# Optimization experiments

Measured on AMD Instinct MI355X. Metric: run time of the kernel, lower is better.

The kernel has to match this reference:

```python
import jax, jax.numpy as jnp
import numpy as np

SEQ_LEN = 1024
BATCH = 256
HIDDEN = 100
OUT = 1

L_FILTER = [-0.0106, 0.0329, 0.0308, -0.187, -0.028, 0.6309, 0.7148, 0.2304]
H_FILTER = [-0.2304, 0.7148, -0.6309, -0.028, 0.187, 0.0308, -0.0329, -0.0106]


def _create_W(P, is_l, rng):
    filt = L_FILTER if is_l else H_FILTER
    eps = np.min(np.abs(filt))
    W = rng.standard_normal((P, P)) * 0.1 * eps
    for i in range(P):
        for k, j in enumerate(range(i, min(i + len(filt), P))):
            W[i, j] = filt[k]
    return jnp.asarray(W, dtype=jnp.float32)


def setup_inputs() -> dict:
    key = jax.random.key(0)
    ks = jax.random.split(key, 16)
    rng = np.random.default_rng(0)
    T, H = SEQ_LEN, HIDDEN
    s = 1.0 / np.sqrt(H)

    def lstm_params(k):
        k1, k2, k3 = jax.random.split(k, 3)
        Wih = jax.random.uniform(k1, (4 * H, 1), jnp.float32, -s, s)
        Whh = jax.random.uniform(k2, (4 * H, H), jnp.float32, -s, s)
        b = jax.random.uniform(k3, (4 * H,), jnp.float32, -s, s)
        return Wih, Whh, b

    Wih1, Whh1, b1 = lstm_params(ks[0])
    Wih2, Whh2, b2 = lstm_params(ks[1])
    Wih3, Whh3, b3 = lstm_params(ks[2])
    return {
        "x": jax.random.normal(ks[3], (BATCH, T, 1), jnp.float32),
        "W1H": _create_W(T, False, rng),
        "b1H": jax.random.uniform(ks[4], (T,), jnp.float32, -1 / np.sqrt(T), 1 / np.sqrt(T)),
        "W1L": _create_W(T, True, rng),
        "b1L": jax.random.uniform(ks[5], (T,), jnp.float32, -1 / np.sqrt(T), 1 / np.sqrt(T)),
        "W2H": _create_W(T // 2, False, rng),
        "b2H": jax.random.uniform(ks[6], (T // 2,), jnp.float32, -1 / np.sqrt(T // 2), 1 / np.sqrt(T // 2)),
        "W2L": _create_W(T // 2, True, rng),
        "b2L": jax.random.uniform(ks[7], (T // 2,), jnp.float32, -1 / np.sqrt(T // 2), 1 / np.sqrt(T // 2)),
        "Wih1": Wih1, "Whh1": Whh1, "b1": b1,
        "Wih2": Wih2, "Whh2": Whh2, "b2": b2,
        "Wih3": Wih3, "Whh3": Whh3, "b3": b3,
        "Wout": jax.random.uniform(ks[8], (OUT, H), jnp.float32, -s, s),
        "bout": jax.random.uniform(ks[9], (OUT,), jnp.float32, -s, s),
    }


def _avgpool2(x):  # [B, L] -> [B, L//2], AvgPool1d(kernel=2, stride=2)
    B, L = x.shape
    return x.reshape(B, L // 2, 2).mean(-1)


def _lstm(x, Wih, Whh, b):
    # x: [B, T, 1]; torch LSTM gate order i, f, g, o; h0 = c0 = 0
    H = Whh.shape[1]
    gx = jnp.einsum('bti,gi->btg', x, Wih) + b  # [B, T, 4H]

    def step(carry, g):
        h, c = carry
        z = g + h @ Whh.T
        i, f, gg, o = jnp.split(z, 4, axis=-1)
        c = jax.nn.sigmoid(f) * c + jax.nn.sigmoid(i) * jnp.tanh(gg)
        h = jax.nn.sigmoid(o) * jnp.tanh(c)
        return (h, c), h

    B = x.shape[0]
    h0 = jnp.zeros((B, H), x.dtype)
    _, hs = jax.lax.scan(step, (h0, h0), jnp.swapaxes(gx, 0, 1))
    return jnp.swapaxes(hs, 0, 1)  # [B, T, H]


def reference(x, W1H, b1H, W1L, b1L, W2H, b2H, W2L, b2L,
              Wih1, Whh1, b1, Wih2, Whh2, b2, Wih3, Whh3, b3, Wout, bout):
    inp = x[:, :, -1]  # [B, T]
    ah1 = jax.nn.sigmoid(inp @ W1H.T + b1H)
    al1 = jax.nn.sigmoid(inp @ W1L.T + b1L)
    xh1 = _avgpool2(ah1)  # [B, T/2]
    xl1 = _avgpool2(al1)  # [B, T/2]
    ah2 = jax.nn.sigmoid(xl1 @ W2H.T + b2H)
    al2 = jax.nn.sigmoid(xl1 @ W2L.T + b2L)
    xh2 = _avgpool2(ah2)  # [B, T/4]
    xl2 = _avgpool2(al2)  # [B, T/4]
    s1 = _lstm(xh1[..., None], Wih1, Whh1, b1)
    s2 = _lstm(xh2[..., None], Wih2, Whh2, b2)
    s3 = _lstm(xl2[..., None], Wih3, Whh3, b3)
    cat = jnp.concatenate([s1, s2, s3], axis=1)  # [B, T, H]
    out = cat @ Wout.T + bout  # [B, T, OUT]
    return out[:, -1, :]
```

## Files before the change

kernel.cpp:

```cpp
#include <hip/hip_runtime.h>
#include <math.h>

typedef __bf16 bf16x8 __attribute__((ext_vector_type(8)));
typedef _Float16 f16x8 __attribute__((ext_vector_type(8)));
typedef _Float16 f16x4 __attribute__((ext_vector_type(4)));
typedef float f32x4 __attribute__((ext_vector_type(4)));

__device__ __forceinline__ unsigned short f2bf(float f) {
  unsigned int u = __builtin_bit_cast(unsigned int, f);
  u += 0x7fffu + ((u >> 16) & 1u);
  return (unsigned short)(u >> 16);
}
__device__ __forceinline__ unsigned int pack2bf(float a, float b) {
  return (unsigned int)f2bf(a) | ((unsigned int)f2bf(b) << 16);
}

#define GK_PAD2 72
template <int WFP32, int XFP32>
__global__ __launch_bounds__(256) void gemm_mfma_sig_pool(
    const void* __restrict__ Wv, const float* __restrict__ bias,
    const void* __restrict__ Xv, void* __restrict__ Y,
    int K, int Np, int out_bf16) {
  __shared__ unsigned short Wt[64][GK_PAD2];
  __shared__ unsigned short Xt[16][GK_PAD2];
  const int tid = threadIdx.x;
  const int i_base = blockIdx.x * 64;
  const int b_base = blockIdx.y * 16;
  const int srow = tid >> 2, sseg = tid & 3;
  const int xr = tid >> 4, xs = tid & 15;
  const int wv = tid >> 6, lane = tid & 63;
  const int L15 = lane & 15, q = lane >> 4;

  const float* Wf = (const float*)Wv;
  const float* Xf = (const float*)Xv;
  const unsigned short* Wh = (const unsigned short*)Wv;
  const unsigned short* Xh = (const unsigned short*)Xv;

  float4 wf[2][4];
  uint4 wh[2][2];
  float4 xf[2];
  uint2 xh2[2];

#define LOADW(S, KO)                                                          \
  do {                                                                        \
    if (WFP32) {                                                              \
      _Pragma("unroll") for (int j = 0; j < 4; j++)                           \
          wf[S][j] = *(const float4*)&Wf[(size_t)(i_base + srow) * K + (KO) + \
                                         sseg * 16 + 4 * j];                  \
    } else {                                                                  \
      _Pragma("unroll") for (int j = 0; j < 2; j++)                           \
          wh[S][j] = *(const uint4*)&Wh[(size_t)(i_base + srow) * K + (KO) +  \
                                        sseg * 16 + 8 * j];                   \
    }                                                                         \
  } while (0)

#define LOADX(S, KO)                                                          \
  do {                                                                        \
    if (XFP32) {                                                              \
      xf[S] = *(const float4*)&Xf[(size_t)(b_base + xr) * K + (KO) + xs * 4]; \
    } else {                                                                  \
      xh2[S] = *(const uint2*)&Xh[(size_t)(b_base + xr) * K + (KO) + xs * 4]; \
    }                                                                         \
  } while (0)

#define STAGEW(S)                                                             \
  do {                                                                        \
    if (WFP32) {                                                              \
      uint4 p0 = {pack2bf(wf[S][0].x, wf[S][0].y),                            \
                  pack2bf(wf[S][0].z, wf[S][0].w),                            \
                  pack2bf(wf[S][1].x, wf[S][1].y),                            \
                  pack2bf(wf[S][1].z, wf[S][1].w)};                           \
      uint4 p1 = {pack2bf(wf[S][2].x, wf[S][2].y),                            \
                  pack2bf(wf[S][2].z, wf[S][2].w),                            \
                  pack2bf(wf[S][3].x, wf[S][3].y),                            \
                  pack2bf(wf[S][3].z, wf[S][3].w)};                           \
      *(uint4*)&Wt[srow][sseg * 16] = p0;                                     \
      *(uint4*)&Wt[srow][sseg * 16 + 8] = p1;                                 \
    } else {                                                                  \
      *(uint4*)&Wt[srow][sseg * 16] = wh[S][0];                               \
      *(uint4*)&Wt[srow][sseg * 16 + 8] = wh[S][1];                           \
    }                                                                         \
  } while (0)

#define STAGEX(S)                                                             \
  do {                                                                        \
    if (XFP32) {                                                              \
      uint2 p = {pack2bf(xf[S].x, xf[S].y), pack2bf(xf[S].z, xf[S].w)};       \
      *(uint2*)&Xt[xr][xs * 4] = p;                                           \
    } else {                                                                  \
      *(uint2*)&Xt[xr][xs * 4] = xh2[S];                                      \
    }                                                                         \
  } while (0)

#define DOMFMA                                                                \
  do {                                                                        \
    _Pragma("unroll") for (int kt = 0; kt < 2; kt++) {                        \
      bf16x8 a = *(const bf16x8*)&Wt[wv * 16 + L15][kt * 32 + q * 8];         \
      bf16x8 b = *(const bf16x8*)&Xt[L15][kt * 32 + q * 8];                   \
      acc = __builtin_amdgcn_mfma_f32_16x16x32_bf16(a, b, acc, 0, 0, 0);      \
    }                                                                         \
  } while (0)

  f32x4 acc = {};
  LOADW(0, 0);
  LOADX(0, 0);
  for (int k0 = 0; k0 < K; k0 += 128) {
    LOADW(1, k0 + 64);
    LOADX(1, k0 + 64);
    STAGEW(0);
    STAGEX(0);
    __syncthreads();
    DOMFMA;
    __syncthreads();
    if (k0 + 128 < K) {
      LOADW(0, k0 + 128);
      LOADX(0, k0 + 128);
    }
    STAGEW(1);
    STAGEX(1);
    __syncthreads();
    DOMFMA;
    __syncthreads();
  }
#undef LOADW
#undef LOADX
#undef STAGEW
#undef STAGEX
#undef DOMFMA

  {
    const int nrow = i_base + 16 * wv + q * 4;
    const float bi0 = bias[nrow], bi1 = bias[nrow + 1];
    const float bi2 = bias[nrow + 2], bi3 = bias[nrow + 3];
    const int b = b_base + L15;
    const float a0 = __builtin_amdgcn_rcpf(1.f + __expf(-(acc[0] + bi0)));
    const float a1 = __builtin_amdgcn_rcpf(1.f + __expf(-(acc[1] + bi1)));
    const float a2 = __builtin_amdgcn_rcpf(1.f + __expf(-(acc[2] + bi2)));
    const float a3 = __builtin_amdgcn_rcpf(1.f + __expf(-(acc[3] + bi3)));
    const float p0 = 0.5f * (a0 + a1), p1 = 0.5f * (a2 + a3);
    const int pidx = nrow >> 1;
    if (out_bf16) {
      *(unsigned int*)&((unsigned short*)Y)[(size_t)b * Np + pidx] = pack2bf(p0, p1);
    } else {
      *(float2*)&((float*)Y)[(size_t)b * Np + pidx] = make_float2(p0, p1);
    }
  }
}

#define LOG2E 1.44269504f
#define TWOL2E 2.88539008f
__global__ __launch_bounds__(256) void prep_whh(
    const float* __restrict__ Whh, const float* __restrict__ b3,
    _Float16* __restrict__ P) {
  const int idx = blockIdx.x * 256 + threadIdx.x;
  if (idx >= 400 * 16) return;
  const int row = idx >> 4, ch = idx & 15;
  const int hid = row >> 2, gate = row & 3;
  const int src = gate * 100 + hid;
  const float s = (gate == 2) ? TWOL2E : LOG2E;
  f16x8 v;
#pragma unroll
  for (int j = 0; j < 8; j++) {
    const int k = ch * 8 + j;
    float f = 0.f;
    if (k < 100) f = Whh[(size_t)src * 100 + k] * s;
    v[j] = (_Float16)f;
  }
  *(f16x8*)&P[(size_t)row * 128 + ch * 8] = v;
}

#define TSTEPS 256

__device__ __forceinline__ float qb0(float x) {
  return __builtin_bit_cast(float, __builtin_amdgcn_mov_dpp(__builtin_bit_cast(int, x), 0x00, 0xf, 0xf, true));
}
__device__ __forceinline__ float qb1(float x) {
  return __builtin_bit_cast(float, __builtin_amdgcn_mov_dpp(__builtin_bit_cast(int, x), 0x55, 0xf, 0xf, true));
}
__device__ __forceinline__ float qb2(float x) {
  return __builtin_bit_cast(float, __builtin_amdgcn_mov_dpp(__builtin_bit_cast(int, x), 0xAA, 0xf, 0xf, true));
}
__device__ __forceinline__ float qb3(float x) {
  return __builtin_bit_cast(float, __builtin_amdgcn_mov_dpp(__builtin_bit_cast(int, x), 0xFF, 0xf, 0xf, true));
}

__global__ __launch_bounds__(512, 2) void lstm_mfma(
    const float* __restrict__ X, const _Float16* __restrict__ P,
    const float* __restrict__ Whh, const float* __restrict__ Wih,
    const float* __restrict__ b3, const float* __restrict__ Wout,
    const float* __restrict__ bout, float* __restrict__ out) {
  const int bat = blockIdx.x;
  const int t = threadIdx.x;
  const int w = t >> 6, lane = t & 63;
  const int quad = lane >> 4, c = lane & 15;
  const int TB = (w == 7) ? 21 : w * 3;
  const int NT = (w == 7) ? 4 : 3;

  __shared__ __align__(16) _Float16 hbuf[2][128];
  __shared__ float xrow[TSTEPS];
  __shared__ float red[128];

  for (int i = t; i < TSTEPS; i += 512) xrow[i] = X[(size_t)bat * TSTEPS + i];
  if (t < 128) { hbuf[0][t] = (_Float16)0.f; hbuf[1][t] = (_Float16)0.f; }

#define LDA(J, KT) const f16x8 A##J##KT = \
    *(const f16x8*)&P[(size_t)((TB + J) * 16 + c) * 128 + (KT) * 32 + quad * 8];
  LDA(0,0) LDA(0,1) LDA(0,2)
  LDA(1,0) LDA(1,1) LDA(1,2)
  LDA(2,0) LDA(2,1) LDA(2,2)
  LDA(3,0) LDA(3,1) LDA(3,2)
#undef LDA

  const bool act = (c < 4 * NT);
  const int J = c >> 2, g = c & 3;
  const int myhid = 4 * (TB + (act ? J : 0)) + quad;
  const int grow = g * 100 + myhid;
  const float sc = (g == 2) ? TWOL2E : LOG2E;
  const float u_ = Wih[grow] * sc;
  const float bz = b3[grow] * sc;
  const float4 wt0 = *(const float4*)&Whh[(size_t)grow * 100 + 96];
  const float4 wt = make_float4(wt0.x * sc, wt0.y * sc, wt0.z * sc, wt0.w * sc);
  const float mm = (g == 2) ? 2.f : 1.f;
  const float dd = (g == 2) ? -1.f : 0.f;
  float cst = 0.f;
  __syncthreads();

#define SIG2(zz) __builtin_amdgcn_rcpf(1.f + __builtin_amdgcn_exp2f(-(zz)))
#define STEPB(HC, HN, XT)                                                      \
  {                                                                            \
    const _Float16* hc = (HC);                                                 \
    const f16x8 B0 = *(const f16x8*)&hc[0 * 32 + quad * 8];                    \
    const f16x8 B1 = *(const f16x8*)&hc[1 * 32 + quad * 8];                    \
    const f16x8 B2 = *(const f16x8*)&hc[2 * 32 + quad * 8];                    \
    f32x4 z0 = {0.f,0.f,0.f,0.f}, z1 = z0, z2 = z0, z3 = z0;                   \
    { f32x4 za = z0, zb = z0;                                                  \
      za = __builtin_amdgcn_mfma_f32_16x16x32_f16(A00, B0, za, 0, 0, 0);       \
      zb = __builtin_amdgcn_mfma_f32_16x16x32_f16(A01, B1, zb, 0, 0, 0);       \
      za = __builtin_amdgcn_mfma_f32_16x16x32_f16(A02, B2, za, 0, 0, 0);       \
      z0 = za + zb; }                                                          \
    { f32x4 za = {0.f,0.f,0.f,0.f}, zb = za;                                   \
      za = __builtin_amdgcn_mfma_f32_16x16x32_f16(A10, B0, za, 0, 0, 0);       \
      zb = __builtin_amdgcn_mfma_f32_16x16x32_f16(A11, B1, zb, 0, 0, 0);       \
      za = __builtin_amdgcn_mfma_f32_16x16x32_f16(A12, B2, za, 0, 0, 0);       \
      z1 = za + zb; }                                                          \
    { f32x4 za = {0.f,0.f,0.f,0.f}, zb = za;                                   \
      za = __builtin_amdgcn_mfma_f32_16x16x32_f16(A20, B0, za, 0, 0, 0);       \
      zb = __builtin_amdgcn_mfma_f32_16x16x32_f16(A21, B1, zb, 0, 0, 0);       \
      za = __builtin_amdgcn_mfma_f32_16x16x32_f16(A22, B2, za, 0, 0, 0);       \
      z2 = za + zb; }                                                          \
    if (w == 7) {                                                              \
      f32x4 za = {0.f,0.f,0.f,0.f}, zb = za;                                   \
      za = __builtin_amdgcn_mfma_f32_16x16x32_f16(A30, B0, za, 0, 0, 0);       \
      zb = __builtin_amdgcn_mfma_f32_16x16x32_f16(A31, B1, zb, 0, 0, 0);       \
      za = __builtin_amdgcn_mfma_f32_16x16x32_f16(A32, B2, za, 0, 0, 0);       \
      z3 = za + zb; }                                                          \
    if (act) {                                                                 \
      const f32x4 zt = (J == 0) ? z0 : (J == 1) ? z1 : (J == 2) ? z2 : z3;     \
      float zs = (g == 0) ? zt[0] : (g == 1) ? zt[1] : (g == 2) ? zt[2] : zt[3];\
      const f16x4 ht = *(const f16x4*)&hc[96];                                 \
      zs = fmaf(wt.x, (float)ht[0], zs);                                       \
      zs = fmaf(wt.y, (float)ht[1], zs);                                       \
      zs = fmaf(wt.z, (float)ht[2], zs);                                       \
      zs = fmaf(wt.w, (float)ht[3], zs);                                       \
      zs = fmaf(u_, (XT), zs + bz);                                            \
      const float a = mm * SIG2(zs) + dd;                                      \
      const float ai = qb0(a), af = qb1(a), ag = qb2(a), ao = qb3(a);          \
      cst = fmaf(af, cst, ai * ag);                                            \
      const float th = 2.f * SIG2(TWOL2E * cst) - 1.f;                         \
      if (g == 0) (HN)[myhid] = (_Float16)(ao * th);                           \
    }                                                                          \
    __syncthreads();                                                           \
  }

  for (int step = 0; step < TSTEPS; step += 2) {
    STEPB(hbuf[0], hbuf[1], xrow[step]);
    STEPB(hbuf[1], hbuf[0], xrow[step + 1]);
  }
#undef STEPB
#undef SIG2

  if (t < 128) {
    float a = 0.f;
    if (t < 100) a = (float)hbuf[0][t] * Wout[t];
    red[t] = a;
  }
  __syncthreads();
  if (t == 0) {
    float s = 0.f;
#pragma unroll
    for (int k = 0; k < 128; k++) s += red[k];
    out[bat] = s + bout[0];
  }
}

extern "C" void kernel_launch(void* const* d_in, const int* in_sizes, int n_in,
                              void* d_out, int out_size, void* d_ws, size_t ws_size,
                              hipStream_t stream) {
  const float* x    = (const float*)d_in[0];
  const float* W1L  = (const float*)d_in[3];
  const float* b1L  = (const float*)d_in[4];
  const float* W2L  = (const float*)d_in[7];
  const float* b2L  = (const float*)d_in[8];
  const float* Wih3 = (const float*)d_in[15];
  const float* Whh3 = (const float*)d_in[16];
  const float* b3   = (const float*)d_in[17];
  const float* Wout = (const float*)d_in[18];
  const float* bout = (const float*)d_in[19];
  float* out = (float*)d_out;

  unsigned short* xl1b = (unsigned short*)d_ws;
  float* xl2 = (float*)(xl1b + (size_t)256 * 512);
  _Float16* P = (_Float16*)(xl2 + (size_t)256 * 256);

  prep_whh<<<25, 256, 0, stream>>>(Whh3, b3, P);
  gemm_mfma_sig_pool<1, 1><<<dim3(16, 16), 256, 0, stream>>>(W1L, b1L, x, xl1b, 1024, 512, 1);
  gemm_mfma_sig_pool<1, 0><<<dim3(8, 16), 256, 0, stream>>>(W2L, b2L, xl1b, xl2, 512, 256, 0);
  lstm_mfma<<<256, 512, 0, stream>>>(xl2, P, Whh3, Wih3, b3, Wout, bout, out);
}
```

Before: 231.1 us.

## Fuse all four kernels into one cooperative kernel with grid syncs

Replaces the four separate launches (Whh prep, two GEMM+sigmoid+pool stages, LSTM) with a single cooperative kernel that separates phases with grid-wide syncs. The GEMM phase now uses 512 threads with a 128-wide K tile and splits K across wave pairs, reducing the partials through shared memory. The aim is to remove launch gaps and inter-kernel drain. In exchange it adds grid.sync costs, limits the grid to what can be co-resident, and idles half the blocks during the second GEMM.

```diff
diff --git a/kernel.cpp b/kernel.cpp
--- a/kernel.cpp
+++ b/kernel.cpp
@@ -1,11 +1,18 @@
 #include <hip/hip_runtime.h>
+#include <hip/hip_cooperative_groups.h>
 #include <math.h>
+
+namespace cg = cooperative_groups;
 
 typedef __bf16 bf16x8 __attribute__((ext_vector_type(8)));
 typedef _Float16 f16x8 __attribute__((ext_vector_type(8)));
 typedef _Float16 f16x4 __attribute__((ext_vector_type(4)));
 typedef float f32x4 __attribute__((ext_vector_type(4)));
 
+#define LOG2E 1.44269504f
+#define TWOL2E 2.88539008f
+#define TSTEPS 256
+
 __device__ __forceinline__ unsigned short f2bf(float f) {
   unsigned int u = __builtin_bit_cast(unsigned int, f);
   u += 0x7fffu + ((u >> 16) & 1u);
@@ -15,43 +22,54 @@
   return (unsigned int)f2bf(a) | ((unsigned int)f2bf(b) << 16);
 }
 
-#define GK_PAD2 72
-template <int WFP32, int XFP32>
-__global__ __launch_bounds__(256) void gemm_mfma_sig_pool(
-    const void* __restrict__ Wv, const float* __restrict__ bias,
+__device__ __forceinline__ float qb0(float x) {
+  return __builtin_bit_cast(float, __builtin_amdgcn_mov_dpp(__builtin_bit_cast(int, x), 0x00, 0xf, 0xf, true));
+}
+__device__ __forceinline__ float qb1(float x) {
+  return __builtin_bit_cast(float, __builtin_amdgcn_mov_dpp(__builtin_bit_cast(int, x), 0x55, 0xf, 0xf, true));
+}
+__device__ __forceinline__ float qb2(float x) {
+  return __builtin_bit_cast(float, __builtin_amdgcn_mov_dpp(__builtin_bit_cast(int, x), 0xAA, 0xf, 0xf, true));
+}
+__device__ __forceinline__ float qb3(float x) {
+  return __builtin_bit_cast(float, __builtin_amdgcn_mov_dpp(__builtin_bit_cast(int, x), 0xFF, 0xf, 0xf, true));
+}
+
+struct SmemG {
+  unsigned short Wt[64][136];
+  unsigned short Xt[16][136];
+  float racc[4][64][4];
+};
+struct SmemL {
+  _Float16 hbuf[2][128];
+  float xrow[TSTEPS];
+  float red[128];
+};
+union SmemU { SmemG g; SmemL l; };
+
+template <int XFP32>
+__device__ __forceinline__ void gemm_phase(
+    const float* __restrict__ Wf, const float* __restrict__ bias,
     const void* __restrict__ Xv, void* __restrict__ Y,
-    int K, int Np, int out_bf16) {
-  __shared__ unsigned short Wt[64][GK_PAD2];
-  __shared__ unsigned short Xt[16][GK_PAD2];
-  const int tid = threadIdx.x;
-  const int i_base = blockIdx.x * 64;
-  const int b_base = blockIdx.y * 16;
-  const int srow = tid >> 2, sseg = tid & 3;
-  const int xr = tid >> 4, xs = tid & 15;
-  const int wv = tid >> 6, lane = tid & 63;
+    const int K, const int Np, const int out_bf16,
+    const int i_base, const int b_base, SmemG* sm, const int tid) {
+  const int srow = tid >> 3, sseg = tid & 7;
+  const int xr = tid >> 5, xs = tid & 31;
+  const int w = tid >> 6, lane = tid & 63;
+  const int rgrp = w >> 1, kg = w & 1;
   const int L15 = lane & 15, q = lane >> 4;
-
-  const float* Wf = (const float*)Wv;
   const float* Xf = (const float*)Xv;
-  const unsigned short* Wh = (const unsigned short*)Wv;
   const unsigned short* Xh = (const unsigned short*)Xv;
 
   float4 wf[2][4];
-  uint4 wh[2][2];
   float4 xf[2];
   uint2 xh2[2];
 
 #define LOADW(S, KO)                                                          \
   do {                                                                        \
-    if (WFP32) {                                                              \
-      _Pragma("unroll") for (int j = 0; j < 4; j++)                           \
-          wf[S][j] = *(const float4*)&Wf[(size_t)(i_base + srow) * K + (KO) + \
-                                         sseg * 16 + 4 * j];                  \
-    } else {                                                                  \
-      _Pragma("unroll") for (int j = 0; j < 2; j++)                           \
-          wh[S][j] = *(const uint4*)&Wh[(size_t)(i_base + srow) * K + (KO) +  \
-                                        sseg * 16 + 8 * j];                   \
-    }                                                                         \
+    _Pragma("unroll") for (int j = 0; j < 4; j++)                             \
+        wf[S][j] = *(const float4*)&Wf[(size_t)(i_base + srow) * K + (KO) +   \
+                                       sseg * 16 + 4 * j];                    \
   } while (0)
 
 #define LOADX(S, KO)                                                          \
@@ -65,56 +83,52 @@
 
 #define STAGEW(S)                                                             \
   do {                                                                        \
-    if (WFP32) {                                                              \
-      uint4 p0 = {pack2bf(wf[S][0].x, wf[S][0].y),                            \
-                  pack2bf(wf[S][0].z, wf[S][0].w),                            \
-                  pack2bf(wf[S][1].x, wf[S][1].y),                            \
-                  pack2bf(wf[S][1].z, wf[S][1].w)};                           \
-      uint4 p1 = {pack2bf(wf[S][2].x, wf[S][2].y),                            \
-                  pack2bf(wf[S][2].z, wf[S][2].w),                            \
-                  pack2bf(wf[S][3].x, wf[S][3].y),                            \
-                  pack2bf(wf[S][3].z, wf[S][3].w)};                           \
-      *(uint4*)&Wt[srow][sseg * 16] = p0;                                     \
-      *(uint4*)&Wt[srow][sseg * 16 + 8] = p1;                                 \
-    } else {                                                                  \
-      *(uint4*)&Wt[srow][sseg * 16] = wh[S][0];                               \
-      *(uint4*)&Wt[srow][sseg * 16 + 8] = wh[S][1];                           \
-    }                                                                         \
+    uint4 p0 = {pack2bf(wf[S][0].x, wf[S][0].y),                              \
+                pack2bf(wf[S][0].z, wf[S][0].w),                              \
+                pack2bf(wf[S][1].x, wf[S][1].y),                              \
+                pack2bf(wf[S][1].z, wf[S][1].w)};                             \
+    uint4 p1 = {pack2bf(wf[S][2].x, wf[S][2].y),                              \
+                pack2bf(wf[S][2].z, wf[S][2].w),                              \
+                pack2bf(wf[S][3].x, wf[S][3].y),                              \
+                pack2bf(wf[S][3].z, wf[S][3].w)};                             \
+    *(uint4*)&sm->Wt[srow][sseg * 16] = p0;                                   \
+    *(uint4*)&sm->Wt[srow][sseg * 16 + 8] = p1;                               \
   } while (0)
 
 #define STAGEX(S)                                                             \
   do {                                                                        \
     if (XFP32) {                                                              \
       uint2 p = {pack2bf(xf[S].x, xf[S].y), pack2bf(xf[S].z, xf[S].w)};       \
-      *(uint2*)&Xt[xr][xs * 4] = p;                                           \
+      *(uint2*)&sm->Xt[xr][xs * 4] = p;                                       \
     } else {                                                                  \
-      *(uint2*)&Xt[xr][xs * 4] = xh2[S];                                      \
+      *(uint2*)&sm->Xt[xr][xs * 4] = xh2[S];                                  \
     }                                                                         \
   } while (0)
 
 #define DOMFMA                                                                \
   do {                                                                        \
-    _Pragma("unroll") for (int kt = 0; kt < 2; kt++) {                        \
-      bf16x8 a = *(const bf16x8*)&Wt[wv * 16 + L15][kt * 32 + q * 8];         \
-      bf16x8 b = *(const bf16x8*)&Xt[L15][kt * 32 + q * 8];                   \
-      acc = __builtin_amdgcn_mfma_f32_16x16x32_bf16(a, b, acc, 0, 0, 0);      \
+    _Pragma("unroll") for (int tki = 0; tki < 2; tki++) {                     \
+      const int kt = kg * 2 + tki;                                            \
+      bf16x8 a = *(const bf16x8*)&sm->Wt[rgrp * 16 + L15][kt * 32 + q * 8];   \
+      bf16x8 bb = *(const bf16x8*)&sm->Xt[L15][kt * 32 + q * 8];              \
+      acc = __builtin_amdgcn_mfma_f32_16x16x32_bf16(a, bb, acc, 0, 0, 0);     \
     }                                                                         \
   } while (0)
 
   f32x4 acc = {};
   LOADW(0, 0);
   LOADX(0, 0);
-  for (int k0 = 0; k0 < K; k0 += 128) {
-    LOADW(1, k0 + 64);
-    LOADX(1, k0 + 64);
+  for (int k0 = 0; k0 < K; k0 += 256) {
+    LOADW(1, k0 + 128);
+    LOADX(1, k0 + 128);
     STAGEW(0);
     STAGEX(0);
     __syncthreads();
     DOMFMA;
     __syncthreads();
-    if (k0 + 128 < K) {
-      LOADW(0, k0 + 128);
-      LOADX(0, k0 + 128);
+    if (k0 + 256 < K) {
+      LOADW(0, k0 + 256);
+      LOADX(0, k0 + 256);
     }
     STAGEW(1);
     STAGEX(1);
@@ -128,8 +142,11 @@
 #undef STAGEX
 #undef DOMFMA
 
-  {
-    const int nrow = i_base + 16 * wv + q * 4;
+  if (kg == 1) *(f32x4*)&sm->racc[rgrp][lane][0] = acc;
+  __syncthreads();
+  if (kg == 0) {
+    acc += *(const f32x4*)&sm->racc[rgrp][lane][0];
+    const int nrow = i_base + rgrp * 16 + q * 4;
     const float bi0 = bias[nrow], bi1 = bias[nrow + 1];
     const float bi2 = bias[nrow + 2], bi3 = bias[nrow + 3];
     const int b = b_base + L15;
@@ -145,85 +162,90 @@
       *(float2*)&((float*)Y)[(size_t)b * Np + pidx] = make_float2(p0, p1);
     }
   }
-}
-
-#define LOG2E 1.44269504f
-#define TWOL2E 2.88539008f
-__global__ __launch_bounds__(256) void prep_whh(
+  __syncthreads();
+}
+
+__global__ __launch_bounds__(512, 2) void fused_all(
+    const float* __restrict__ x, const float* __restrict__ W1L,
+    const float* __restrict__ b1L, const float* __restrict__ W2L,
+    const float* __restrict__ b2L, const float* __restrict__ Wih,
     const float* __restrict__ Whh, const float* __restrict__ b3,
-    _Float16* __restrict__ P) {
-  const int idx = blockIdx.x * 256 + threadIdx.x;
-  if (idx >= 400 * 16) return;
-  const int row = idx >> 4, ch = idx & 15;
-  const int hid = row >> 2, gate = row & 3;
-  const int src = gate * 100 + hid;
-  const float s = (gate == 2) ? TWOL2E : LOG2E;
-  f16x8 v;
+    const float* __restrict__ Wout, const float* __restrict__ bout,
+    unsigned short* __restrict__ xl1b, float* __restrict__ xl2,
+    _Float16* __restrict__ P, float* __restrict__ out) {
+  __shared__ __align__(16) SmemU smem;
+  const int t = threadIdx.x;
+  const int blk = blockIdx.x;
+  cg::grid_group grid = cg::this_grid();
+
+  {
+    const int idx = blk * 512 + t;
+    if (idx < 400 * 16) {
+      const int row = idx >> 4, ch = idx & 15;
+      const int hid = row >> 2, gate = row & 3;
+      const int src = gate * 100 + hid;
+      const float s = (gate == 2) ? TWOL2E : LOG2E;
+      f16x8 v;
 #pragma unroll
-  for (int j = 0; j < 8; j++) {
-    const int k = ch * 8 + j;
-    float f = 0.f;
-    if (k < 100) f = Whh[(size_t)src * 100 + k] * s;
-    v[j] = (_Float16)f;
-  }
-  *(f16x8*)&P[(size_t)row * 128 + ch * 8] = v;
-}
-
-#define TSTEPS 256
-
-__device__ __forceinline__ float qb0(float x) {
-  return __builtin_bit_cast(float, __builtin_amdgcn_mov_dpp(__builtin_bit_cast(int, x), 0x00, 0xf, 0xf, true));
-}
-__device__ __forceinline__ float qb1(float x) {
-  return __builtin_bit_cast(float, __builtin_amdgcn_mov_dpp(__builtin_bit_cast(int, x), 0x55, 0xf, 0xf, true));
-}
-__device__ __forceinline__ float qb2(float x) {
-  return __builtin_bit_cast(float, __builtin_amdgcn_mov_dpp(__builtin_bit_cast(int, x), 0xAA, 0xf, 0xf, true));
-}
-__device__ __forceinline__ float qb3(float x) {
-  return __builtin_bit_cast(float, __builtin_amdgcn_mov_dpp(__builtin_bit_cast(int, x), 0xFF, 0xf, 0xf, true));
-}
-
-__global__ __launch_bounds__(512, 2) void lstm_mfma(
-    const float* __restrict__ X, const _Float16* __restrict__ P,
-    const float* __restrict__ Whh, const float* __restrict__ Wih,
-    const float* __restrict__ b3, const float* __restrict__ Wout,
-    const float* __restrict__ bout, float* __restrict__ out) {
-  const int bat = blockIdx.x;
-  const int t = threadIdx.x;
-  const int w = t >> 6, lane = t & 63;
-  const int quad = lane >> 4, c = lane & 15;
-  const int TB = (w == 7) ? 21 : w * 3;
-  const int NT = (w == 7) ? 4 : 3;
-
-  __shared__ __align__(16) _Float16 hbuf[2][128];
-  __shared__ float xrow[TSTEPS];
-  __shared__ float red[128];
-
-  for (int i = t; i < TSTEPS; i += 512) xrow[i] = X[(size_t)bat * TSTEPS + i];
-  if (t < 128) { hbuf[0][t] = (_Float16)0.f; hbuf[1][t] = (_Float16)0.f; }
+      for (int j = 0; j < 8; j++) {
+        const int k = ch * 8 + j;
+        float f = 0.f;
+        if (k < 100) f = Whh[(size_t)src * 100 + k] * s;
+        v[j] = (_Float16)f;
+      }
+      *(f16x8*)&P[(size_t)row * 128 + ch * 8] = v;
+    }
+  }
+  __threadfence();
+  grid.sync();
+
+  gemm_phase<1>(W1L, b1L, x, xl1b, 1024, 512, 1,
+                (blk >> 4) * 64, (blk & 15) * 16, &smem.g, t);
+  __threadfence();
+  grid.sync();
+
+  if (blk < 128)
+    gemm_phase<0>(W2L, b2L, xl1b, xl2, 512, 256, 0,
+                  (blk >> 4) * 64, (blk & 15) * 16, &smem.g, t);
+  __threadfence();
+  grid.sync();
+
+  {
+    const int bat = blk;
+    const int w = t >> 6, lane = t & 63;
+    const int quad = lane >> 4, c = lane & 15;
+    const int TB = (w == 7) ? 21 : w * 3;
+    const int NT = (w == 7) ? 4 : 3;
+
+    _Float16* h0 = smem.l.hbuf[0];
+    _Float16* h1 = smem.l.hbuf[1];
+    float* xrow = smem.l.xrow;
+    float* red = smem.l.red;
+
+    for (int i = t; i < TSTEPS; i += 512) xrow[i] = xl2[(size_t)bat * TSTEPS + i];
+    if (t < 128) { h0[t] = (_Float16)0.f; h1[t] = (_Float16)0.f; }
 
 #define LDA(J, KT) const f16x8 A##J##KT = \
     *(const f16x8*)&P[(size_t)((TB + J) * 16 + c) * 128 + (KT) * 32 + quad * 8];
-  LDA(0,0) LDA(0,1) LDA(0,2)
-  LDA(1,0) LDA(1,1) LDA(1,2)
-  LDA(2,0) LDA(2,1) LDA(2,2)
-  LDA(3,0) LDA(3,1) LDA(3,2)
+    LDA(0,0) LDA(0,1) LDA(0,2)
+    LDA(1,0) LDA(1,1) LDA(1,2)
+    LDA(2,0) LDA(2,1) LDA(2,2)
+    LDA(3,0) LDA(3,1) LDA(3,2)
 #undef LDA
 
-  const bool act = (c < 4 * NT);
-  const int J = c >> 2, g = c & 3;
-  const int myhid = 4 * (TB + (act ? J : 0)) + quad;
-  const int grow = g * 100 + myhid;
-  const float sc = (g == 2) ? TWOL2E : LOG2E;
-  const float u_ = Wih[grow] * sc;
-  const float bz = b3[grow] * sc;
-  const float4 wt0 = *(const float4*)&Whh[(size_t)grow * 100 + 96];
-  const float4 wt = make_float4(wt0.x * sc, wt0.y * sc, wt0.z * sc, wt0.w * sc);
-  const float mm = (g == 2) ? 2.f : 1.f;
-  const float dd = (g == 2) ? -1.f : 0.f;
-  float cst = 0.f;
-  __syncthreads();
+    const bool act = (c < 4 * NT);
+    const int J = c >> 2, g = c & 3;
+    const int myhid = 4 * (TB + (act ? J : 0)) + quad;
+    const int grow = g * 100 + myhid;
+    const float sc = (g == 2) ? TWOL2E : LOG2E;
+    const float u_ = Wih[grow] * sc;
+    const float bz = b3[grow] * sc;
+    const float4 wt0 = *(const float4*)&Whh[(size_t)grow * 100 + 96];
+    const float4 wt = make_float4(wt0.x * sc, wt0.y * sc, wt0.z * sc, wt0.w * sc);
+    const float mm = (g == 2) ? 2.f : 1.f;
+    const float dd = (g == 2) ? -1.f : 0.f;
+    float cst = 0.f;
+    __syncthreads();
 
 #define SIG2(zz) __builtin_amdgcn_rcpf(1.f + __builtin_amdgcn_exp2f(-(zz)))
 #define STEPB(HC, HN, XT)                                                      \
@@ -272,24 +294,25 @@
     __syncthreads();                                                           \
   }
 
-  for (int step = 0; step < TSTEPS; step += 2) {
-    STEPB(hbuf[0], hbuf[1], xrow[step]);
-    STEPB(hbuf[1], hbuf[0], xrow[step + 1]);
-  }
+    for (int step = 0; step < TSTEPS; step += 2) {
+      STEPB(h0, h1, xrow[step]);
+      STEPB(h1, h0, xrow[step + 1]);
+    }
 #undef STEPB
 #undef SIG2
 
-  if (t < 128) {
-    float a = 0.f;
-    if (t < 100) a = (float)hbuf[0][t] * Wout[t];
-    red[t] = a;
-  }
-  __syncthreads();
-  if (t == 0) {
-    float s = 0.f;
+    if (t < 128) {
+      float a = 0.f;
+      if (t < 100) a = (float)h0[t] * Wout[t];
+      red[t] = a;
+    }
+    __syncthreads();
+    if (t == 0) {
+      float s = 0.f;
 #pragma unroll
-    for (int k = 0; k < 128; k++) s += red[k];
-    out[bat] = s + bout[0];
+      for (int k = 0; k < 128; k++) s += red[k];
+      out[bat] = s + bout[0];
+    }
   }
 }
 
@@ -312,8 +335,7 @@
   float* xl2 = (float*)(xl1b + (size_t)256 * 512);
   _Float16* P = (_Float16*)(xl2 + (size_t)256 * 256);
 
-  prep_whh<<<25, 256, 0, stream>>>(Whh3, b3, P);
-  gemm_mfma_sig_pool<1, 1><<<dim3(16, 16), 256, 0, stream>>>(W1L, b1L, x, xl1b, 1024, 512, 1);
-  gemm_mfma_sig_pool<1, 0><<<dim3(8, 16), 256, 0, stream>>>(W2L, b2L, xl1b, xl2, 512, 256, 0);
-  lstm_mfma<<<256, 512, 0, stream>>>(xl2, P, Whh3, Wih3, b3, Wout, bout, out);
-}
+  void* args[] = {&x, &W1L, &b1L, &W2L, &b2L, &Wih3, &Whh3, &b3,
+                  &Wout, &bout, &xl1b, &xl2, &P, &out};
+  hipLaunchCooperativeKernel(fused_all, dim3(256), dim3(512), args, 0u, stream);
+}
```

New measurement: 449.3 us. 1.94x slower.

## Fold Whh prep into first GEMM launch and double-buffer LDS with one sync

Applied to the files above, without the earlier changes.

Removes the separate prep_whh launch by adding an extra column of blocks (blockIdx.x==16) to the first GEMM grid that perform the Whh fp16 repacking. The GEMM K-loop now uses two LDS buffers so that staging the next tile overlaps the MFMA on the current one, cutting the barriers per 64-wide K step from two to one. This saves one kernel launch and some synchronisation overhead in exchange for doubled shared memory per block. The LSTM kernel, which most likely dominates the runtime, is unchanged.

```diff
diff --git a/kernel.cpp b/kernel.cpp
--- a/kernel.cpp
+++ b/kernel.cpp
@@ -6,6 +6,9 @@
 typedef _Float16 f16x4 __attribute__((ext_vector_type(4)));
 typedef float f32x4 __attribute__((ext_vector_type(4)));
 
+#define LOG2E 1.44269504f
+#define TWOL2E 2.88539008f
+
 __device__ __forceinline__ unsigned short f2bf(float f) {
   unsigned int u = __builtin_bit_cast(unsigned int, f);
   u += 0x7fffu + ((u >> 16) & 1u);
@@ -16,13 +19,35 @@
 }
 
 #define GK_PAD2 72
-template <int WFP32, int XFP32>
+template <int WFP32, int XFP32, int DO_PREP>
 __global__ __launch_bounds__(256) void gemm_mfma_sig_pool(
     const void* __restrict__ Wv, const float* __restrict__ bias,
     const void* __restrict__ Xv, void* __restrict__ Y,
-    int K, int Np, int out_bf16) {
-  __shared__ unsigned short Wt[64][GK_PAD2];
-  __shared__ unsigned short Xt[16][GK_PAD2];
+    int K, int Np, int out_bf16,
+    const float* __restrict__ Whh, const float* __restrict__ b3,
+    _Float16* __restrict__ P) {
+  if (DO_PREP && blockIdx.x == 16) {
+    const int base = blockIdx.y * 256 + threadIdx.x;
+    for (int idx = base; idx < 400 * 16; idx += 4096) {
+      const int row = idx >> 4, ch = idx & 15;
+      const int hid = row >> 2, gate = row & 3;
+      const int src = gate * 100 + hid;
+      const float s = (gate == 2) ? TWOL2E : LOG2E;
+      f16x8 v;
+#pragma unroll
+      for (int j = 0; j < 8; j++) {
+        const int k = ch * 8 + j;
+        float f = 0.f;
+        if (k < 100) f = Whh[(size_t)src * 100 + k] * s;
+        v[j] = (_Float16)f;
+      }
+      *(f16x8*)&P[(size_t)row * 128 + ch * 8] = v;
+    }
+    return;
+  }
+
+  __shared__ unsigned short Wt[2][64][GK_PAD2];
+  __shared__ unsigned short Xt[2][16][GK_PAD2];
   const int tid = threadIdx.x;
   const int i_base = blockIdx.x * 64;
   const int b_base = blockIdx.y * 16;
@@ -63,7 +88,7 @@
     }                                                                         \
   } while (0)
 
-#define STAGEW(S)                                                             \
+#define STAGEW(S, PB)                                                         \
   do {                                                                        \
     if (WFP32) {                                                              \
       uint4 p0 = {pack2bf(wf[S][0].x, wf[S][0].y),                            \
@@ -74,54 +99,53 @@
                   pack2bf(wf[S][2].z, wf[S][2].w),                            \
                   pack2bf(wf[S][3].x, wf[S][3].y),                            \
                   pack2bf(wf[S][3].z, wf[S][3].w)};                           \
-      *(uint4*)&Wt[srow][sseg * 16] = p0;                                     \
-      *(uint4*)&Wt[srow][sseg * 16 + 8] = p1;                                 \
+      *(uint4*)&Wt[PB][srow][sseg * 16] = p0;                                 \
+      *(uint4*)&Wt[PB][srow][sseg * 16 + 8] = p1;                             \
     } else {                                                                  \
-      *(uint4*)&Wt[srow][sseg * 16] = wh[S][0];                               \
-      *(uint4*)&Wt[srow][sseg * 16 + 8] = wh[S][1];                           \
-    }                                                                         \
-  } while (0)
-
-#define STAGEX(S)                                                             \
+      *(uint4*)&Wt[PB][srow][sseg * 16] = wh[S][0];                           \
+      *(uint4*)&Wt[PB][srow][sseg * 16 + 8] = wh[S][1];                       \
+    }                                                                         \
+  } while (0)
+
+#define STAGEX(S, PB)                                                         \
   do {                                                                        \
     if (XFP32) {                                                              \
       uint2 p = {pack2bf(xf[S].x, xf[S].y), pack2bf(xf[S].z, xf[S].w)};       \
-      *(uint2*)&Xt[xr][xs * 4] = p;                                           \
+      *(uint2*)&Xt[PB][xr][xs * 4] = p;                                       \
     } else {                                                                  \
-      *(uint2*)&Xt[xr][xs * 4] = xh2[S];                                      \
-    }                                                                         \
-  } while (0)
-
-#define DOMFMA                                                                \
+      *(uint2*)&Xt[PB][xr][xs * 4] = xh2[S];                                  \
+    }                                                                         \
+  } while (0)
+
+#define DOMFMA(PB)                                                            \
   do {                                                                        \
     _Pragma("unroll") for (int kt = 0; kt < 2; kt++) {                        \
-      bf16x8 a = *(const bf16x8*)&Wt[wv * 16 + L15][kt * 32 + q * 8];         \
-      bf16x8 b = *(const bf16x8*)&Xt[L15][kt * 32 + q * 8];                   \
+      bf16x8 a = *(const bf16x8*)&Wt[PB][wv * 16 + L15][kt * 32 + q * 8];     \
+      bf16x8 b = *(const bf16x8*)&Xt[PB][L15][kt * 32 + q * 8];               \
       acc = __builtin_amdgcn_mfma_f32_16x16x32_bf16(a, b, acc, 0, 0, 0);      \
     }                                                                         \
   } while (0)
 
   f32x4 acc = {};
+  const int S = K >> 6;
   LOADW(0, 0);
   LOADX(0, 0);
-  for (int k0 = 0; k0 < K; k0 += 128) {
-    LOADW(1, k0 + 64);
-    LOADX(1, k0 + 64);
-    STAGEW(0);
-    STAGEX(0);
+  STAGEW(0, 0);
+  STAGEX(0, 0);
+  LOADW(1, 64);
+  LOADX(1, 64);
+  __syncthreads();
+  for (int s = 1; s < S; s++) {
+    STAGEW(s & 1, s & 1);
+    STAGEX(s & 1, s & 1);
+    if (s + 1 < S) {
+      LOADW((s + 1) & 1, 64 * (s + 1));
+      LOADX((s + 1) & 1, 64 * (s + 1));
+    }
+    DOMFMA((s - 1) & 1);
     __syncthreads();
-    DOMFMA;
-    __syncthreads();
-    if (k0 + 128 < K) {
-      LOADW(0, k0 + 128);
-      LOADX(0, k0 + 128);
-    }
-    STAGEW(1);
-    STAGEX(1);
-    __syncthreads();
-    DOMFMA;
-    __syncthreads();
-  }
+  }
+  DOMFMA((S - 1) & 1);
 #undef LOADW
 #undef LOADX
 #undef STAGEW
@@ -145,28 +169,6 @@
       *(float2*)&((float*)Y)[(size_t)b * Np + pidx] = make_float2(p0, p1);
     }
   }
-}
-
-#define LOG2E 1.44269504f
-#define TWOL2E 2.88539008f
-__global__ __launch_bounds__(256) void prep_whh(
-    const float* __restrict__ Whh, const float* __restrict__ b3,
-    _Float16* __restrict__ P) {
-  const int idx = blockIdx.x * 256 + threadIdx.x;
-  if (idx >= 400 * 16) return;
-  const int row = idx >> 4, ch = idx & 15;
-  const int hid = row >> 2, gate = row & 3;
-  const int src = gate * 100 + hid;
-  const float s = (gate == 2) ? TWOL2E : LOG2E;
-  f16x8 v;
-#pragma unroll
-  for (int j = 0; j < 8; j++) {
-    const int k = ch * 8 + j;
-    float f = 0.f;
-    if (k < 100) f = Whh[(size_t)src * 100 + k] * s;
-    v[j] = (_Float16)f;
-  }
-  *(f16x8*)&P[(size_t)row * 128 + ch * 8] = v;
 }
 
 #define TSTEPS 256
@@ -312,8 +314,9 @@
   float* xl2 = (float*)(xl1b + (size_t)256 * 512);
   _Float16* P = (_Float16*)(xl2 + (size_t)256 * 256);
 
-  prep_whh<<<25, 256, 0, stream>>>(Whh3, b3, P);
-  gemm_mfma_sig_pool<1, 1><<<dim3(16, 16), 256, 0, stream>>>(W1L, b1L, x, xl1b, 1024, 512, 1);
-  gemm_mfma_sig_pool<1, 0><<<dim3(8, 16), 256, 0, stream>>>(W2L, b2L, xl1b, xl2, 512, 256, 0);
+  gemm_mfma_sig_pool<1, 1, 1><<<dim3(17, 16), 256, 0, stream>>>(
+      W1L, b1L, x, xl1b, 1024, 512, 1, Whh3, b3, P);
+  gemm_mfma_sig_pool<1, 0, 0><<<dim3(8, 16), 256, 0, stream>>>(
+      W2L, b2L, xl1b, xl2, 512, 256, 0, nullptr, nullptr, nullptr);
   lstm_mfma<<<256, 512, 0, stream>>>(xl2, P, Whh3, Wih3, b3, Wout, bout, out);
 }
```

Result: slower. 271.0 us (+17.2%).
